# Kernel tuning notes

Hardware: AMD Instinct MI355X
Metric: run time of the kernel (lower is better)

Reference implementation:

```python
import jax, jax.numpy as jnp
import numpy as np
import math

B, S, D, H = 2, 2048, 1024, 16
DK = D // H  # 64


def _rope_tables(seq_len, dim):
    # matches RotaryEmbedding: inv_freq over arange(0, dim, 2)/dim
    inv_freq = 1.0 / (10000.0 ** (jnp.arange(0, dim, 2, dtype=jnp.float32) / dim))
    pos = jnp.arange(seq_len, dtype=jnp.float32)
    freqs = pos[:, None] * inv_freq[None, :]  # [S, dim/2]
    return jnp.cos(freqs), jnp.sin(freqs)


def _apply_rope(x, cos, sin):
    # x: [B, S, H, DK]; cos/sin: [S, DK/2] -> broadcast over heads
    cos = cos[:, None, :]
    sin = sin[:, None, :]
    t = x.shape[-1] // 2
    x1, x2 = x[..., :t], x[..., t:]
    return jnp.concatenate([x1 * cos - x2 * sin, x1 * sin + x2 * cos], axis=-1)


def setup_inputs() -> dict:
    key = jax.random.key(0)
    ks = jax.random.split(key, 12)
    sc = 1.0 / math.sqrt(D)
    inp = {
        'q': jax.random.normal(ks[0], (B, S, D), jnp.float32),
        'k': jax.random.normal(ks[1], (B, S, D), jnp.float32),
        'v': jax.random.normal(ks[2], (B, S, D), jnp.float32),
        'mask': jnp.tril(jnp.ones((S, S), jnp.int32))[None, None, :, :],  # causal [1,1,S,S]
        'Wq': jax.random.normal(ks[3], (D, D), jnp.float32) * sc,
        'bq': jnp.zeros((D,), jnp.float32),
        'Wk': jax.random.normal(ks[4], (D, D), jnp.float32) * sc,
        'bk': jnp.zeros((D,), jnp.float32),
        'Wv': jax.random.normal(ks[5], (D, D), jnp.float32) * sc,
        'bv': jnp.zeros((D,), jnp.float32),
        'Wo': jax.random.normal(ks[6], (D, D), jnp.float32) * sc,
        'bo': jnp.zeros((D,), jnp.float32),
    }
    return inp


def reference(q, k, v, mask, Wq, bq, Wk, bk, Wv, bv, Wo, bo):
    b, sq, _ = q.shape
    sk = k.shape[1]
    # QKV projections (torch Linear: x @ W^T + b), split heads
    qh = (q @ Wq.T + bq).reshape(b, sq, H, DK)
    kh = (k @ Wk.T + bk).reshape(b, sk, H, DK)
    vh = (v @ Wv.T + bv).reshape(b, sk, H, DK)
    # RoPE on q and k
    cos_q, sin_q = _rope_tables(sq, DK)
    cos_k, sin_k = _rope_tables(sk, DK)
    qh = _apply_rope(qh, cos_q, sin_q)
    kh = _apply_rope(kh, cos_k, sin_k)
    # masked softmax attention: [B,H,Sq,Sk]
    scores = jnp.einsum('bqhd,bkhd->bhqk', qh, kh) / math.sqrt(DK)
    scores = jnp.where(mask == 0, jnp.float32(-10000.0), scores)
    attn = jax.nn.softmax(scores, axis=-1)
    out = jnp.einsum('bhqk,bkhd->bqhd', attn, vh).reshape(b, sq, D)
    return out @ Wo.T + bo
```

## Files before the change

### kernel.cpp

```cpp
#include <hip/hip_runtime.h>
#include <hip/hip_bf16.h>
#include <math.h>

#define BB  2
#define SS  2048
#define DD  1024
#define HH  16
#define DKK 64

typedef __attribute__((ext_vector_type(8))) short bfrag;
typedef __attribute__((ext_vector_type(4))) float f32x4;

__device__ __forceinline__ unsigned short f2bf(float x) {
    union { float f; unsigned u; } v; v.f = x;
    unsigned r = v.u + 0x7FFF + ((v.u >> 16) & 1);
    return (unsigned short)(r >> 16);
}
__device__ __forceinline__ unsigned pk2(float a, float b) {
    union { __hip_bfloat162 h; unsigned u; } v;
    v.h = __float22bfloat162_rn(float2{a, b});
    return v.u;
}
__device__ __forceinline__ void async16(const void* g, void* l) {
    __builtin_amdgcn_global_load_lds(
        (const __attribute__((address_space(1))) void*)g,
        (__attribute__((address_space(3))) void*)l, 16, 0, 0);
}

__constant__ int JQT[48] = {
 15,14,30,27,25,30,22,26,
 31,29,28,28,26,12,23,20,
 31,29,13,27,25,23,11,21,
 16,19,20,10,24,24,21, 9,
 16,17,18,17, 8, 6,22,18,
  0, 1, 2, 3, 4, 5, 7,19};
__constant__ int JKLO[48] = {
  0, 0, 0, 0, 0,15,11,13,
  0, 0,14, 0, 0, 0,12,10,
 16,15, 0,14,13, 0, 0,11,
  8, 0, 0, 0,12, 0, 0, 0,
  0, 0, 0, 9, 0, 0, 0, 9,
  0, 0, 0, 0, 0, 0, 0,10};
__constant__ int JPART[48] = {
 0,0,1,1,1,2,2,2,
 1,1,2,1,1,0,2,2,
 2,2,0,2,2,1,0,2,
 2,1,1,0,2,1,1,0,
 1,1,1,2,0,0,1,2,
 0,0,0,0,0,0,0,2};

__global__ __launch_bounds__(256)
void cvt_all(const float* __restrict__ q, const float* __restrict__ k,
             const float* __restrict__ v, const float* __restrict__ wq,
             const float* __restrict__ wk, const float* __restrict__ wv,
             const float* __restrict__ wo, unsigned short* __restrict__ ws)
{
    int b = blockIdx.x;
    const float* src; unsigned short* dst;
    const size_t MI = 1048576;
    if      (b <  4096) { src = q;  dst = ws;           }
    else if (b <  8192) { src = k;  dst = ws + 4*MI;  b -= 4096;  }
    else if (b < 12288) { src = v;  dst = ws + 8*MI;  b -= 8192;  }
    else if (b < 13312) { src = wq; dst = ws + 12*MI; b -= 12288; }
    else if (b < 14336) { src = wk; dst = ws + 13*MI; b -= 13312; }
    else if (b < 15360) { src = wv; dst = ws + 14*MI; b -= 14336; }
    else                { src = wo; dst = ws + 15*MI; b -= 15360; }
    size_t off = (size_t)b * 1024 + threadIdx.x * 4;
    float4 x = *(const float4*)(src + off);
    uint2 o = { pk2(x.x, x.y), pk2(x.z, x.w) };
    *(uint2*)(dst + off) = o;
}

__global__ __launch_bounds__(256, 3)
void gemm_qkv(const unsigned short* __restrict__ qA, const unsigned short* __restrict__ kA,
              const unsigned short* __restrict__ vA, const unsigned short* __restrict__ Wqb,
              const unsigned short* __restrict__ Wkb, const unsigned short* __restrict__ Wvb,
              const float* __restrict__ bq, const float* __restrict__ bk,
              const float* __restrict__ bv,
              unsigned short* __restrict__ qo, unsigned short* __restrict__ ko,
              unsigned short* __restrict__ vo)
{
    __shared__ unsigned short As[128 * 32];
    __shared__ unsigned short Bs[128 * 32];

    const int wsel = blockIdx.z;
    const unsigned short* A = (wsel == 0) ? qA : (wsel == 1) ? kA : vA;
    const unsigned short* W = (wsel == 0) ? Wqb : (wsel == 1) ? Wkb : Wvb;
    const float* bias       = (wsel == 0) ? bq : (wsel == 1) ? bk : bv;
    unsigned short* outp    = (wsel == 0) ? qo : (wsel == 1) ? ko : vo;

    const int t = threadIdx.x, w = t >> 6, lane = t & 63;
    const int lq = lane & 15, quad = lane >> 4;
    const int m0 = blockIdx.y * 128, n0 = blockIdx.x * 128;
    const int wm = (w >> 1) * 64, wn = (w & 1) * 64;
    const int srow = lane >> 2, sch = lane & 3;

    f32x4 acc[4][4] = {};

    for (int kt = 0; kt < 32; ++kt) {
        const int kofs = kt * 32;
        #pragma unroll
        for (int p = 0; p < 2; ++p) {
            const int rb = (p * 4 + w) * 16;
            async16(A + (size_t)(m0 + rb + srow) * 1024 + kofs + sch * 8,
                    (char*)As + (p * 4 + w) * 1024);
            async16(W + (size_t)(n0 + rb + srow) * 1024 + kofs + sch * 8,
                    (char*)Bs + (p * 4 + w) * 1024);
        }
        __syncthreads();
        bfrag a[4], b[4];
        #pragma unroll
        for (int i = 0; i < 4; ++i)
            a[i] = *(const bfrag*)&As[(wm + i * 16 + lq) * 32 + quad * 8];
        #pragma unroll
        for (int j = 0; j < 4; ++j)
            b[j] = *(const bfrag*)&Bs[(wn + j * 16 + lq) * 32 + quad * 8];
        #pragma unroll
        for (int i = 0; i < 4; ++i)
            #pragma unroll
            for (int j = 0; j < 4; ++j)
                acc[i][j] = __builtin_amdgcn_mfma_f32_16x16x32_bf16(a[i], b[j], acc[i][j], 0, 0, 0);
        __syncthreads();
    }

    if (wsel == 2) {
        #pragma unroll
        for (int j = 0; j < 4; ++j) {
            const int n = n0 + wn + j * 16 + lq;
            const int hh = n >> 6, d = n & 63;
            const float bj = bias[n];
            #pragma unroll
            for (int i = 0; i < 4; ++i) {
                const int m = m0 + wm + i * 16 + quad * 4;
                const int bb2 = m >> 11, sb = m & (SS - 1);
                uint2 pk = { pk2(acc[i][j][0] + bj, acc[i][j][1] + bj),
                             pk2(acc[i][j][2] + bj, acc[i][j][3] + bj) };
                *(uint2*)(outp + ((size_t)((bb2 * HH + hh) * DKK + d)) * SS + sb) = pk;
            }
        }
    } else {
        const float osc = (wsel == 0) ? 0.18033688011112042f : 1.0f;
        #pragma unroll
        for (int jc = 0; jc < 2; ++jc) {
            const int n1 = n0 + wn + jc * 16 + lq;
            const float b1 = bias[n1], b2 = bias[n1 + 32];
            const int ifq = jc * 16 + lq;
            const int hh = n1 >> 6;
            const float inv_rev = exp2f(-(float)ifq * 0.4152410118609203f) * 0.15915494309189535f;
            #pragma unroll
            for (int i = 0; i < 4; ++i)
                #pragma unroll
                for (int r = 0; r < 4; ++r) {
                    const int m = m0 + wm + i * 16 + quad * 4 + r;
                    const int bb2 = m >> 11, s = m & (SS - 1);
                    float rev = (float)s * inv_rev;
                    rev -= floorf(rev);
                    const float sn = __builtin_amdgcn_sinf(rev);
                    const float cs = __builtin_amdgcn_cosf(rev);
                    const float va = acc[i][jc][r] + b1;
                    const float vb = acc[i][jc + 2][r] + b2;
                    const size_t base = (((size_t)(bb2 * HH + hh)) * SS + s) * DKK;
                    outp[base + ifq]      = f2bf((va * cs - vb * sn) * osc);
                    outp[base + ifq + 32] = f2bf((va * sn + vb * cs) * osc);
                }
        }
    }
}

#define FM 20.0f
__global__ __launch_bounds__(256, 6)
void attn_mfma(const unsigned short* __restrict__ qh,
               const unsigned short* __restrict__ kh,
               const unsigned short* __restrict__ vt,
               unsigned short* __restrict__ ao,
               float* __restrict__ pO, float* __restrict__ pml)
{
    __shared__ unsigned short Ks[2 * 64 * 32];
    __shared__ unsigned short Vt[2 * 64 * 32];
    __shared__ unsigned short Ps[64 * 72];

    const int t = threadIdx.x, w = t >> 6, lane = t & 63;
    const int lq = lane & 15, quad = lane >> 4;
    const int srow = lane >> 2, sch = lane & 3;

    const int g  = blockIdx.x + 256 * blockIdx.y;
    const int bh = g & 31;
    const int w5 = g >> 5;
    const int qtx  = JQT[w5];
    const int klo  = JKLO[w5];
    const int part = JPART[w5];
    const int kthi = (part == 1) ? (((qtx + 1) >> 1) - 1) : qtx;
    const int q0 = qtx * 64;
    const size_t bhq = (size_t)bh * SS * DKK;

    bfrag qb[2];
    #pragma unroll
    for (int h = 0; h < 2; ++h)
        qb[h] = *(const bfrag*)(qh + bhq +
            (size_t)(q0 + w * 16 + lq) * 64 + h * 32 + quad * 8);

    f32x4 o[4] = {};
    float lst = 0.f;

    for (int kt = klo; kt <= kthi; ++kt) {
        const int k0 = kt * 64;
        __syncthreads();
        #pragma unroll
        for (int h = 0; h < 2; ++h) {
            async16(kh + bhq + (size_t)(k0 + w * 16 + srow) * 64 + h * 32 + sch * 8,
                    (char*)&Ks[h * 64 * 32 + w * 16 * 32]);
            async16(vt + bhq + (size_t)(w * 16 + srow) * SS + k0 + h * 32 + sch * 8,
                    (char*)&Vt[h * 64 * 32 + w * 16 * 32]);
        }
        __syncthreads();

        f32x4 sc[4] = {};
        #pragma unroll
        for (int j = 0; j < 4; ++j) {
            bfrag kb0 = *(const bfrag*)&Ks[(j * 16 + lq) * 32 + quad * 8];
            bfrag kb1 = *(const bfrag*)&Ks[64 * 32 + (j * 16 + lq) * 32 + quad * 8];
            sc[j] = __builtin_amdgcn_mfma_f32_16x16x32_bf16(kb0, qb[0], sc[j], 0, 0, 0);
            sc[j] = __builtin_amdgcn_mfma_f32_16x16x32_bf16(kb1, qb[1], sc[j], 0, 0, 0);
        }
        if (kt == qtx) {
            const int qg = q0 + w * 16 + lq;
            #pragma unroll
            for (int j = 0; j < 4; ++j)
                #pragma unroll
                for (int r = 0; r < 4; ++r) {
                    const int kg = k0 + j * 16 + quad * 4 + r;
                    if (kg > qg) sc[j][r] = -1e30f;
                }
        }

        #pragma unroll
        for (int j = 0; j < 4; ++j) {
            float p0 = exp2f(sc[j][0] - FM), p1 = exp2f(sc[j][1] - FM);
            float p2 = exp2f(sc[j][2] - FM), p3 = exp2f(sc[j][3] - FM);
            lst += (p0 + p1) + (p2 + p3);
            uint2 pk = { pk2(p0, p1), pk2(p2, p3) };
            *(uint2*)&Ps[(w * 16 + lq) * 72 + j * 16 + quad * 4] = pk;
        }

        bfrag pa0 = *(const bfrag*)&Ps[(w * 16 + lq) * 72 + quad * 8];
        bfrag pa1 = *(const bfrag*)&Ps[(w * 16 + lq) * 72 + 32 + quad * 8];
        #pragma unroll
        for (int j2 = 0; j2 < 4; ++j2) {
            bfrag vb0 = *(const bfrag*)&Vt[(j2 * 16 + lq) * 32 + quad * 8];
            bfrag vb1 = *(const bfrag*)&Vt[64 * 32 + (j2 * 16 + lq) * 32 + quad * 8];
            o[j2] = __builtin_amdgcn_mfma_f32_16x16x32_bf16(pa0, vb0, o[j2], 0, 0, 0);
            o[j2] = __builtin_amdgcn_mfma_f32_16x16x32_bf16(pa1, vb1, o[j2], 0, 0, 0);
        }
    }

    float lt = lst;
    lt += __shfl_xor(lt, 16);
    lt += __shfl_xor(lt, 32);

    if (part == 0) {
        const int b = bh >> 4, hh = bh & 15;
        #pragma unroll
        for (int r = 0; r < 4; ++r) {
            const float li = __shfl(lt, quad * 4 + r);
            const float inv = 1.0f / li;
            const int s = q0 + w * 16 + quad * 4 + r;
            const size_t rowb = ((size_t)(b * SS + s)) * DD + hh * DKK;
            #pragma unroll
            for (int j2 = 0; j2 < 4; ++j2)
                ao[rowb + j2 * 16 + lq] = f2bf(o[j2][r] * inv);
        }
    } else {
        const int pidx = (bh * 16 + (qtx - 16)) * 2 + (part - 1);
        float* po = pO + (size_t)pidx * 4096;
        if (quad == 0)
            pml[pidx * 64 + w * 16 + lq] = lt;
        #pragma unroll
        for (int r = 0; r < 4; ++r)
            #pragma unroll
            for (int j2 = 0; j2 < 4; ++j2)
                po[(w * 16 + quad * 4 + r) * 64 + j2 * 16 + lq] = o[j2][r];
    }
}

__global__ __launch_bounds__(256)
void combine(const float* __restrict__ pO, const float* __restrict__ pml,
             unsigned short* __restrict__ ao)
{
    const int ti = blockIdx.x, bh = blockIdx.y;
    const int qtx = 16 + ti;
    const int p0 = (bh * 16 + ti) * 2;
    const float* O1 = pO + (size_t)p0 * 4096;
    const float* O2 = O1 + 4096;

    const int t = threadIdx.x;
    const int row = t >> 2, c0 = (t & 3) * 16;
    const float l1 = pml[p0 * 64 + row];
    const float l2 = pml[(p0 + 1) * 64 + row];
    const float inv = 1.0f / (l1 + l2);

    const int b = bh >> 4, h = bh & 15;
    const int s = qtx * 64 + row;
    const size_t ob = ((size_t)(b * SS + s)) * DD + h * DKK + c0;
    #pragma unroll
    for (int c = 0; c < 16; c += 4) {
        float4 a = *(const float4*)(O1 + row * 64 + c0 + c);
        float4 d = *(const float4*)(O2 + row * 64 + c0 + c);
        uint2 u = { pk2((a.x + d.x) * inv, (a.y + d.y) * inv),
                    pk2((a.z + d.z) * inv, (a.w + d.w) * inv) };
        *(uint2*)(ao + ob + c) = u;
    }
}

__global__ __launch_bounds__(256, 4)
void gemm_o(const unsigned short* __restrict__ A, const unsigned short* __restrict__ W,
            const float* __restrict__ bias, float* __restrict__ out)
{
    __shared__ unsigned short As[64 * 32];
    __shared__ unsigned short Bs[64 * 32];

    const int t = threadIdx.x, w = t >> 6, lane = t & 63;
    const int lq = lane & 15, quad = lane >> 4;
    const int m0 = blockIdx.y * 64, n0 = blockIdx.x * 64;
    const int wm = (w >> 1) * 32, wn = (w & 1) * 32;
    const int srow = lane >> 2, sch = lane & 3;

    f32x4 acc[2][2] = {};

    for (int kt = 0; kt < 32; ++kt) {
        const int kofs = kt * 32;
        async16(A + (size_t)(m0 + w * 16 + srow) * 1024 + kofs + sch * 8,
                (char*)As + w * 1024);
        async16(W + (size_t)(n0 + w * 16 + srow) * 1024 + kofs + sch * 8,
                (char*)Bs + w * 1024);
        __syncthreads();
        bfrag a[2], b[2];
        #pragma unroll
        for (int i = 0; i < 2; ++i)
            a[i] = *(const bfrag*)&As[(wm + i * 16 + lq) * 32 + quad * 8];
        #pragma unroll
        for (int j = 0; j < 2; ++j)
            b[j] = *(const bfrag*)&Bs[(wn + j * 16 + lq) * 32 + quad * 8];
        #pragma unroll
        for (int i = 0; i < 2; ++i)
            #pragma unroll
            for (int j = 0; j < 2; ++j)
                acc[i][j] = __builtin_amdgcn_mfma_f32_16x16x32_bf16(a[i], b[j], acc[i][j], 0, 0, 0);
        __syncthreads();
    }

    #pragma unroll
    for (int j = 0; j < 2; ++j) {
        const int n = n0 + wn + j * 16 + lq;
        const float bj = bias[n];
        #pragma unroll
        for (int i = 0; i < 2; ++i)
            #pragma unroll
            for (int r = 0; r < 4; ++r) {
                const int m = m0 + wm + i * 16 + quad * 4 + r;
                out[(size_t)m * DD + n] = acc[i][j][r] + bj;
            }
    }
}

extern "C" void kernel_launch(void* const* d_in, const int* in_sizes, int n_in,
                              void* d_out, int out_size, void* d_ws, size_t ws_size,
                              hipStream_t stream)
{
    const float* q  = (const float*)d_in[0];
    const float* k  = (const float*)d_in[1];
    const float* v  = (const float*)d_in[2];
    const float* Wq = (const float*)d_in[4];
    const float* bq = (const float*)d_in[5];
    const float* Wk = (const float*)d_in[6];
    const float* bk = (const float*)d_in[7];
    const float* Wv = (const float*)d_in[8];
    const float* bv = (const float*)d_in[9];
    const float* Wo = (const float*)d_in[10];
    const float* bo = (const float*)d_in[11];
    float* out = (float*)d_out;

    unsigned short* ws = (unsigned short*)d_ws;
    const size_t MI = 1048576;
    unsigned short* qbf = ws;
    unsigned short* kbf = ws + 4 * MI;
    unsigned short* vbf = ws + 8 * MI;
    unsigned short* Wqb = ws + 12 * MI;
    unsigned short* Wkb = ws + 13 * MI;
    unsigned short* Wvb = ws + 14 * MI;
    unsigned short* Wob = ws + 15 * MI;
    unsigned short* qhp = ws + 16 * MI;
    unsigned short* khp = ws + 20 * MI;
    unsigned short* vtp = ws + 24 * MI;
    unsigned short* aop = ws + 28 * MI;
    float* pO  = (float*)ws;
    float* pml = (float*)(ws + 12 * MI);

    const dim3 blk(256);

    cvt_all<<<dim3(16384), blk, 0, stream>>>(q, k, v, Wq, Wk, Wv, Wo, ws);

    gemm_qkv<<<dim3(8, 32, 3), blk, 0, stream>>>(qbf, kbf, vbf, Wqb, Wkb, Wvb,
                                                 bq, bk, bv, qhp, khp, vtp);

    attn_mfma<<<dim3(256, 6), blk, 0, stream>>>(qhp, khp, vtp, aop, pO, pml);

    combine<<<dim3(16, 32), blk, 0, stream>>>(pO, pml, aop);

    gemm_o<<<dim3(16, 64), blk, 0, stream>>>(aop, Wob, bo, out);
}
```

Before: 231.1 us.

## Use raw exp2, swap QKV grid order, hoist attention pointers, deepen gemm_o K-step

Several small changes land together. exp2f is replaced by the hardware v_exp_f32 builtin in the attention softmax and RoPE. The QKV GEMM grid is transposed so consecutive blocks walk M instead of N, which changes L2 reuse of weights versus activations. Attention K/V load addresses become incrementing pointers instead of being recomputed each iteration, and gemm_o now loads a 64-wide K slab per barrier pair, halving its barrier count at the cost of doubled LDS.

```diff
diff --git a/kernel.cpp b/kernel.cpp
--- a/kernel.cpp
+++ b/kernel.cpp
@@ -20,6 +20,13 @@
     union { __hip_bfloat162 h; unsigned u; } v;
     v.h = __float22bfloat162_rn(float2{a, b});
     return v.u;
+}
+__device__ __forceinline__ float fexp2(float x) {
+#if __has_builtin(__builtin_amdgcn_exp2f)
+    return __builtin_amdgcn_exp2f(x);
+#else
+    float r; asm("v_exp_f32 %0, %1" : "=v"(r) : "v"(x)); return r;
+#endif
 }
 __device__ __forceinline__ void async16(const void* g, void* l) {
     __builtin_amdgcn_global_load_lds(
@@ -91,7 +98,7 @@
 
     const int t = threadIdx.x, w = t >> 6, lane = t & 63;
     const int lq = lane & 15, quad = lane >> 4;
-    const int m0 = blockIdx.y * 128, n0 = blockIdx.x * 128;
+    const int m0 = blockIdx.x * 128, n0 = blockIdx.y * 128;
     const int wm = (w >> 1) * 64, wn = (w & 1) * 64;
     const int srow = lane >> 2, sch = lane & 3;
 
@@ -146,7 +153,7 @@
             const float b1 = bias[n1], b2 = bias[n1 + 32];
             const int ifq = jc * 16 + lq;
             const int hh = n1 >> 6;
-            const float inv_rev = exp2f(-(float)ifq * 0.4152410118609203f) * 0.15915494309189535f;
+            const float inv_rev = fexp2(-(float)ifq * 0.4152410118609203f) * 0.15915494309189535f;
             #pragma unroll
             for (int i = 0; i < 4; ++i)
                 #pragma unroll
@@ -199,19 +206,22 @@
         qb[h] = *(const bfrag*)(qh + bhq +
             (size_t)(q0 + w * 16 + lq) * 64 + h * 32 + quad * 8);
 
+    const unsigned short* kp = kh + bhq + (size_t)(klo * 64 + w * 16 + srow) * 64 + sch * 8;
+    const unsigned short* vp = vt + bhq + (size_t)(w * 16 + srow) * SS + klo * 64 + sch * 8;
+    char* ksl = (char*)&Ks[w * 16 * 32];
+    char* vsl = (char*)&Vt[w * 16 * 32];
+
     f32x4 o[4] = {};
     float lst = 0.f;
 
     for (int kt = klo; kt <= kthi; ++kt) {
-        const int k0 = kt * 64;
-        __syncthreads();
-        #pragma unroll
-        for (int h = 0; h < 2; ++h) {
-            async16(kh + bhq + (size_t)(k0 + w * 16 + srow) * 64 + h * 32 + sch * 8,
-                    (char*)&Ks[h * 64 * 32 + w * 16 * 32]);
-            async16(vt + bhq + (size_t)(w * 16 + srow) * SS + k0 + h * 32 + sch * 8,
-                    (char*)&Vt[h * 64 * 32 + w * 16 * 32]);
-        }
+        __syncthreads();
+        async16(kp,      ksl);
+        async16(kp + 32, ksl + 64 * 64);
+        async16(vp,      vsl);
+        async16(vp + 32, vsl + 64 * 64);
+        kp += 64 * 64;
+        vp += 64;
         __syncthreads();
 
         f32x4 sc[4] = {};
@@ -224,6 +234,7 @@
         }
         if (kt == qtx) {
             const int qg = q0 + w * 16 + lq;
+            const int k0 = kt * 64;
             #pragma unroll
             for (int j = 0; j < 4; ++j)
                 #pragma unroll
@@ -235,8 +246,8 @@
 
         #pragma unroll
         for (int j = 0; j < 4; ++j) {
-            float p0 = exp2f(sc[j][0] - FM), p1 = exp2f(sc[j][1] - FM);
-            float p2 = exp2f(sc[j][2] - FM), p3 = exp2f(sc[j][3] - FM);
+            float p0 = fexp2(sc[j][0] - FM), p1 = fexp2(sc[j][1] - FM);
+            float p2 = fexp2(sc[j][2] - FM), p3 = fexp2(sc[j][3] - FM);
             lst += (p0 + p1) + (p2 + p3);
             uint2 pk = { pk2(p0, p1), pk2(p2, p3) };
             *(uint2*)&Ps[(w * 16 + lq) * 72 + j * 16 + quad * 4] = pk;
@@ -315,8 +326,8 @@
 void gemm_o(const unsigned short* __restrict__ A, const unsigned short* __restrict__ W,
             const float* __restrict__ bias, float* __restrict__ out)
 {
-    __shared__ unsigned short As[64 * 32];
-    __shared__ unsigned short Bs[64 * 32];
+    __shared__ unsigned short As[2 * 64 * 32];
+    __shared__ unsigned short Bs[2 * 64 * 32];
 
     const int t = threadIdx.x, w = t >> 6, lane = t & 63;
     const int lq = lane & 15, quad = lane >> 4;
@@ -326,25 +337,31 @@
 
     f32x4 acc[2][2] = {};
 
-    for (int kt = 0; kt < 32; ++kt) {
-        const int kofs = kt * 32;
-        async16(A + (size_t)(m0 + w * 16 + srow) * 1024 + kofs + sch * 8,
-                (char*)As + w * 1024);
-        async16(W + (size_t)(n0 + w * 16 + srow) * 1024 + kofs + sch * 8,
-                (char*)Bs + w * 1024);
-        __syncthreads();
-        bfrag a[2], b[2];
-        #pragma unroll
-        for (int i = 0; i < 2; ++i)
-            a[i] = *(const bfrag*)&As[(wm + i * 16 + lq) * 32 + quad * 8];
-        #pragma unroll
-        for (int j = 0; j < 2; ++j)
-            b[j] = *(const bfrag*)&Bs[(wn + j * 16 + lq) * 32 + quad * 8];
-        #pragma unroll
-        for (int i = 0; i < 2; ++i)
+    for (int kt = 0; kt < 16; ++kt) {
+        const int kofs = kt * 64;
+        #pragma unroll
+        for (int h = 0; h < 2; ++h) {
+            async16(A + (size_t)(m0 + w * 16 + srow) * 1024 + kofs + h * 32 + sch * 8,
+                    (char*)&As[h * 64 * 32 + w * 16 * 32]);
+            async16(W + (size_t)(n0 + w * 16 + srow) * 1024 + kofs + h * 32 + sch * 8,
+                    (char*)&Bs[h * 64 * 32 + w * 16 * 32]);
+        }
+        __syncthreads();
+        #pragma unroll
+        for (int h = 0; h < 2; ++h) {
+            bfrag a[2], b[2];
+            #pragma unroll
+            for (int i = 0; i < 2; ++i)
+                a[i] = *(const bfrag*)&As[h * 64 * 32 + (wm + i * 16 + lq) * 32 + quad * 8];
             #pragma unroll
             for (int j = 0; j < 2; ++j)
-                acc[i][j] = __builtin_amdgcn_mfma_f32_16x16x32_bf16(a[i], b[j], acc[i][j], 0, 0, 0);
+                b[j] = *(const bfrag*)&Bs[h * 64 * 32 + (wn + j * 16 + lq) * 32 + quad * 8];
+            #pragma unroll
+            for (int i = 0; i < 2; ++i)
+                #pragma unroll
+                for (int j = 0; j < 2; ++j)
+                    acc[i][j] = __builtin_amdgcn_mfma_f32_16x16x32_bf16(a[i], b[j], acc[i][j], 0, 0, 0);
+        }
         __syncthreads();
     }
 
@@ -399,7 +416,7 @@
 
     cvt_all<<<dim3(16384), blk, 0, stream>>>(q, k, v, Wq, Wk, Wv, Wo, ws);
 
-    gemm_qkv<<<dim3(8, 32, 3), blk, 0, stream>>>(qbf, kbf, vbf, Wqb, Wkb, Wvb,
+    gemm_qkv<<<dim3(32, 8, 3), blk, 0, stream>>>(qbf, kbf, vbf, Wqb, Wkb, Wvb,
                                                  bq, bk, bv, qhp, khp, vtp);
 
     attn_mfma<<<dim3(256, 6), blk, 0, stream>>>(qhp, khp, vtp, aop, pO, pml);
```

Result: faster. 221.2 us (-4.3%).
